# Optimization experiments

Measured on AMD Instinct MI355X. Metric: run time of the kernel, lower is better.

## Reference

```python
import jax, jax.numpy as jnp
import numpy as np

L = 8      # n_layers
D = 512    # msa_dim
P = 128    # pair_dim
H = 8      # n_heads
HD = D // H  # head_dim = 64
B = 2
NS = 4
S = 384


def setup_inputs() -> dict:
    key = jax.random.key(0)
    ks = jax.random.split(key, 24)
    def rn(k, shape, s=0.02):
        return jax.random.normal(k, shape, dtype=jnp.float32) * s
    return {
        "msa_repr": jax.random.normal(ks[0], (B, NS, S, D), dtype=jnp.float32),
        "pair_repr": jax.random.normal(ks[1], (B, S, S, P), dtype=jnp.float32),
        # per-layer IPA params, stacked along layer axis
        "Wq": rn(ks[2], (L, D, D)), "bq": jnp.zeros((L, D), jnp.float32),
        "Wk": rn(ks[3], (L, D, D)), "bk": jnp.zeros((L, D), jnp.float32),
        "Wv": rn(ks[4], (L, D, D)), "bv": jnp.zeros((L, D), jnp.float32),
        "Wpb": rn(ks[5], (L, P, H)), "bpb": jnp.zeros((L, H), jnp.float32),
        "Wo": rn(ks[6], (L, D, D)), "bo": jnp.zeros((L, D), jnp.float32),
        # shared backbone_update MLP (applied after every layer)
        "Wb1": rn(ks[7], (D, D)), "bb1": jnp.zeros((D,), jnp.float32),
        "Wb2": rn(ks[8], (D, 6)), "bb2": jnp.zeros((6,), jnp.float32),
        # confidence head
        "Wc1": rn(ks[9], (D, D // 2)), "bc1": jnp.zeros((D // 2,), jnp.float32),
        "Wc2": rn(ks[10], (D // 2, 1)), "bc2": jnp.zeros((1,), jnp.float32),
    }


def reference(msa_repr, pair_repr, Wq, bq, Wk, bk, Wv, bv, Wpb, bpb, Wo, bo,
              Wb1, bb1, Wb2, bb2, Wc1, bc1, Wc2, bc2):
    Bd, n_seqs, Sd, Dm = msa_repr.shape
    x0 = msa_repr[:, 0]                      # [B,S,D] target sequence repr
    coords0 = jnp.zeros((Bd, Sd, 3), msa_repr.dtype)
    inv_sqrt_hd = jnp.asarray(1.0 / np.sqrt(HD), msa_repr.dtype)

    def layer(carry, p):
        x, coords = carry
        wq, bq_, wk, bk_, wv, bv_, wpb, bpb_, wo, bo_ = p
        q = (x @ wq + bq_).reshape(Bd, Sd, H, HD)
        k = (x @ wk + bk_).reshape(Bd, Sd, H, HD)
        v = (x @ wv + bv_).reshape(Bd, Sd, H, HD)
        scores = jnp.einsum('bihd,bjhd->bhij', q, k) * inv_sqrt_hd
        bias = jnp.einsum('bijp,ph->bhij', pair_repr, wpb) + bpb_[None, :, None, None]
        attn = jax.nn.softmax(scores + bias, axis=-1)   # dropout=0 (eval)
        out = jnp.einsum('bhij,bjhd->bihd', attn, v).reshape(Bd, Sd, Dm)
        x = x + out @ wo + bo_                          # residual
        upd = jax.nn.relu(x @ Wb1 + bb1) @ Wb2 + bb2    # [B,S,6]
        coords = coords + upd[..., :3]                  # translation only
        return (x, coords), None

    (x, coords), _ = jax.lax.scan(layer, (x0, coords0),
                                  (Wq, bq, Wk, bk, Wv, bv, Wpb, bpb, Wo, bo))
    confidence = jax.nn.sigmoid(jax.nn.relu(x @ Wc1 + bc1) @ Wc2 + bc2)[..., 0]
    return coords, confidence
```

## Files before the change

### kernel.cpp

```cpp
#include <hip/hip_runtime.h>
#include <math.h>

#define L 8
#define D 512
#define DD (D*D)
#define P 128
#define H 8
#define HD 64
#define B 2
#define NS 4
#define S 384
#define BS (B*S)
#define XN (BS*D)
#define SS ((size_t)S*S)
#define BHSS ((size_t)B*H*S*S)
#define NSLAB 32

typedef short bf16x8 __attribute__((ext_vector_type(8)));
typedef float f32x4 __attribute__((ext_vector_type(4)));

__device__ __forceinline__ unsigned short f2b(float f) {
    unsigned u = __float_as_uint(f);
    unsigned r = (u + 0x7FFF + ((u >> 16) & 1)) >> 16;
    return (unsigned short)r;
}
__device__ __forceinline__ float b2f(unsigned short u) {
    return __uint_as_float(((unsigned)u) << 16);
}

__global__ __launch_bounds__(256) void k_init(const float* __restrict__ msa,
                                              float* __restrict__ x,
                                              unsigned short* __restrict__ xb,
                                              float* __restrict__ part) {
    int idx = blockIdx.x * 256 + threadIdx.x;
    if (idx < XN) {
        int b = idx / (S * D);
        int rem = idx - b * (S * D);
        float v = msa[(size_t)b * NS * S * D + rem];
        x[idx] = v;
        xb[idx] = f2b(v);
    }
    if (idx < NSLAB * BS * 3) part[idx] = 0.f;
}

__global__ __launch_bounds__(256) void k_prep(const float* __restrict__ Wq,
        const float* __restrict__ Wk, const float* __restrict__ Wv,
        const float* __restrict__ Wo, const float* __restrict__ Wb1,
        const float* __restrict__ Wc1, unsigned short* __restrict__ wt) {
    __shared__ float ts[64][65];
    const int z = blockIdx.z;
    const float* src; int N = 512;
    if (z < 8)       src = Wq + (size_t)z * DD;
    else if (z < 16) src = Wk + (size_t)(z - 8) * DD;
    else if (z < 24) src = Wv + (size_t)(z - 16) * DD;
    else if (z < 32) src = Wo + (size_t)(z - 24) * DD;
    else if (z == 32) src = Wb1;
    else { src = Wc1; N = 256; }
    unsigned short* dst = wt + (size_t)z * DD;

    const int n0 = blockIdx.x * 64, k0 = blockIdx.y * 64;
    if (n0 >= N) return;
    const int t = threadIdx.x;
    #pragma unroll
    for (int m = 0; m < 16; m++) {
        int f = t + m * 256;
        int r = f >> 6, c = f & 63;
        ts[r][c] = src[(size_t)(k0 + r) * N + n0 + c];
    }
    __syncthreads();
    #pragma unroll
    for (int m = 0; m < 4; m++) {
        int o4 = t + m * 256;
        int nr = o4 >> 4, k4 = o4 & 15;
        ushort4 pk;
        pk.x = f2b(ts[k4 * 4 + 0][nr]);
        pk.y = f2b(ts[k4 * 4 + 1][nr]);
        pk.z = f2b(ts[k4 * 4 + 2][nr]);
        pk.w = f2b(ts[k4 * 4 + 3][nr]);
        *(ushort4*)&dst[(size_t)(n0 + nr) * 512 + k0 + k4 * 4] = pk;
    }
}

__global__ __launch_bounds__(256) void k_biasm(const float* __restrict__ pair,
        const float* __restrict__ Wpb, const float* __restrict__ bpb,
        unsigned short* __restrict__ bias) {
    __shared__ unsigned short Ws[64][136];
    __shared__ unsigned short Ps[64][136];
    const int t = threadIdx.x;
    const int lane = t & 63, w = t >> 6;
    const int jt = blockIdx.x, i = blockIdx.y, b = blockIdx.z;

    #pragma unroll
    for (int m = 0; m < 8; m++) {
        int f = (t + m * 256) * 4;
        float4 wv = *(const float4*)&Wpb[f];
        int l = f >> 10, rem = f & 1023;
        int k = rem >> 3, h = rem & 7;
        int lh = (l << 3) | h;
        Ws[lh + 0][k] = f2b(wv.x);
        Ws[lh + 1][k] = f2b(wv.y);
        Ws[lh + 2][k] = f2b(wv.z);
        Ws[lh + 3][k] = f2b(wv.w);
    }
    const float* prow = pair + (((size_t)b * S + i) * S + jt * 64) * P;
    #pragma unroll
    for (int m = 0; m < 8; m++) {
        int f = (t + m * 256) * 4;
        int r = f >> 7, c = f & 127;
        float4 pv = *(const float4*)&prow[f];
        ushort4 u;
        u.x = f2b(pv.x); u.y = f2b(pv.y); u.z = f2b(pv.z); u.w = f2b(pv.w);
        *(ushort4*)&Ps[r][c] = u;
    }
    __syncthreads();

    f32x4 acc[4];
    #pragma unroll
    for (int mi = 0; mi < 4; mi++) { acc[mi][0] = 0.f; acc[mi][1] = 0.f; acc[mi][2] = 0.f; acc[mi][3] = 0.f; }
    #pragma unroll
    for (int ks = 0; ks < 4; ks++) {
        bf16x8 bv = *(const bf16x8*)&Ps[w * 16 + (lane & 15)][ks * 32 + (lane >> 4) * 8];
        #pragma unroll
        for (int mi = 0; mi < 4; mi++) {
            bf16x8 av = *(const bf16x8*)&Ws[mi * 16 + (lane & 15)][ks * 32 + (lane >> 4) * 8];
            acc[mi] = __builtin_amdgcn_mfma_f32_16x16x32_bf16(av, bv, acc[mi], 0, 0, 0);
        }
    }
    const int j = jt * 64 + w * 16 + (lane & 15);
    #pragma unroll
    for (int mi = 0; mi < 4; mi++)
        #pragma unroll
        for (int reg = 0; reg < 4; reg++) {
            int lh = mi * 16 + (lane >> 4) * 4 + reg;
            float v = acc[mi][reg] + bpb[lh];
            size_t plane = ((size_t)(lh >> 3) * B + b) * H + (lh & 7);
            bias[plane * SS + (size_t)i * S + j] = f2b(v);
        }
}

#define GEMM32_CORE(Abase, Wbase)                                              \
    f32x4 acc; acc[0] = 0.f; acc[1] = 0.f; acc[2] = 0.f; acc[3] = 0.f;         \
    {                                                                          \
        const unsigned short* pa = &(Abase)[(size_t)(m0 + sr) * 512 + scc];    \
        const unsigned short* pb = &(Wbase)[(size_t)(n0 + sr) * 512 + scc];    \
        int4 ra = *(const int4*)pa;                                            \
        int4 rb = *(const int4*)pb;                                            \
        *(int4*)&As[0][sr][scc] = ra;                                          \
        *(int4*)&Bs[0][sr][scc] = rb;                                          \
        __syncthreads();                                                       \
        int cur = 0;                                                           \
        for (int kt = 0; kt < 512; kt += 64) {                                 \
            if (kt + 64 < 512) {                                               \
                ra = *(const int4*)(pa + kt + 64);                             \
                rb = *(const int4*)(pb + kt + 64);                             \
            }                                                                  \
            _Pragma("unroll")                                                  \
            for (int kk = 0; kk < 2; kk++) {                                   \
                bf16x8 a = *(const bf16x8*)&As[cur][wr * 16 + (lane & 15)][kk * 32 + (lane >> 4) * 8]; \
                bf16x8 bb = *(const bf16x8*)&Bs[cur][wc * 16 + (lane & 15)][kk * 32 + (lane >> 4) * 8]; \
                acc = __builtin_amdgcn_mfma_f32_16x16x32_bf16(a, bb, acc, 0, 0, 0); \
            }                                                                  \
            if (kt + 64 < 512) {                                               \
                *(int4*)&As[cur ^ 1][sr][scc] = ra;                            \
                *(int4*)&Bs[cur ^ 1][sr][scc] = rb;                            \
            }                                                                  \
            __syncthreads();                                                   \
            cur ^= 1;                                                          \
        }                                                                      \
    }

__global__ __launch_bounds__(256) void k_phaseA(const unsigned short* __restrict__ xb,
        const unsigned short* __restrict__ wt,
        const float* __restrict__ bq, const float* __restrict__ bk, const float* __restrict__ bv,
        unsigned short* __restrict__ qbb, unsigned short* __restrict__ kbb,
        unsigned short* __restrict__ vtb,
        const float* __restrict__ bb1, const float* __restrict__ Wb2g,
        float* __restrict__ part, int l) {
    __shared__ unsigned short As[2][32][72];
    __shared__ unsigned short Bs[2][32][72];
    const int t = threadIdx.x, lane = t & 63;
    const int w = t >> 6, wr = w >> 1, wc = w & 1;
    const int z = blockIdx.z;
    const int m0 = blockIdx.y * 32, n0 = blockIdx.x * 32;
    const int sr = t >> 3, scc = (t & 7) * 8;

    const unsigned short* Wt;
    const float* bias;
    if (z == 0)      { Wt = wt + (size_t)l * DD;        bias = bq + l * D; }
    else if (z == 1) { Wt = wt + (size_t)(8 + l) * DD;  bias = bk + l * D; }
    else if (z == 2) { Wt = wt + (size_t)(16 + l) * DD; bias = bv + l * D; }
    else             { Wt = wt + (size_t)32 * DD;       bias = bb1; }

    GEMM32_CORE(xb, Wt)

    const int col = n0 + wc * 16 + (lane & 15);
    const float bcol = bias[col];
    if (z < 3) {
        unsigned short* out = (z == 0) ? qbb : (z == 1) ? kbb : vtb;
        const int h = col >> 6, d = col & 63;
        #pragma unroll
        for (int reg = 0; reg < 4; reg++) {
            int row = m0 + wr * 16 + (lane >> 4) * 4 + reg;
            int b = row / S, i = row - b * S;
            float v = acc[reg] + bcol;
            if (z < 2) out[(((size_t)b * H + h) * S + i) * HD + d] = f2b(v);
            else       out[(((size_t)b * H + h) * HD + d) * S + i] = f2b(v);
        }
    } else {
        const float w20 = Wb2g[col * 6 + 0];
        const float w21 = Wb2g[col * 6 + 1];
        const float w22 = Wb2g[col * 6 + 2];
        #pragma unroll
        for (int reg = 0; reg < 4; reg++) {
            float v = fmaxf(acc[reg] + bcol, 0.f);
            float p0 = v * w20, p1 = v * w21, p2 = v * w22;
            #pragma unroll
            for (int m = 1; m < 16; m <<= 1) {
                p0 += __shfl_xor(p0, m);
                p1 += __shfl_xor(p1, m);
                p2 += __shfl_xor(p2, m);
            }
            if ((lane & 15) == 0) {
                int row = m0 + wr * 16 + (lane >> 4) * 4 + reg;
                float* pp = &part[((size_t)(blockIdx.x * 2 + wc) * BS + row) * 3];
                pp[0] += p0; pp[1] += p1; pp[2] += p2;
            }
        }
    }
}

__global__ __launch_bounds__(256) void k_wo(const unsigned short* __restrict__ aob,
        const unsigned short* __restrict__ wt, const float* __restrict__ bo,
        float* __restrict__ x, unsigned short* __restrict__ xb, int l) {
    __shared__ unsigned short As[2][32][72];
    __shared__ unsigned short Bs[2][32][72];
    const int t = threadIdx.x, lane = t & 63;
    const int w = t >> 6, wr = w >> 1, wc = w & 1;
    const int m0 = blockIdx.y * 32, n0 = blockIdx.x * 32;
    const int sr = t >> 3, scc = (t & 7) * 8;
    const unsigned short* Wt = wt + (size_t)(24 + l) * DD;

    GEMM32_CORE(aob, Wt)

    const int col = n0 + wc * 16 + (lane & 15);
    const float bcol = bo[l * D + col];
    #pragma unroll
    for (int reg = 0; reg < 4; reg++) {
        int row = m0 + wr * 16 + (lane >> 4) * 4 + reg;
        float v = acc[reg] + bcol + x[(size_t)row * D + col];
        x[(size_t)row * D + col] = v;
        xb[(size_t)row * D + col] = f2b(v);
    }
}

__global__ __launch_bounds__(256) void k_final(const unsigned short* __restrict__ xb,
        const unsigned short* __restrict__ wt,
        const float* __restrict__ bb1, const float* __restrict__ Wb2g, float* __restrict__ part,
        const float* __restrict__ bc1, float* __restrict__ hc) {
    __shared__ unsigned short As[2][32][72];
    __shared__ unsigned short Bs[2][32][72];
    const int t = threadIdx.x, lane = t & 63;
    const int w = t >> 6, wr = w >> 1, wc = w & 1;
    const int z = blockIdx.z;
    if (z == 1 && blockIdx.x >= 8) return;
    const int m0 = blockIdx.y * 32, n0 = blockIdx.x * 32;
    const int sr = t >> 3, scc = (t & 7) * 8;
    const unsigned short* Wt = (z == 0) ? wt + (size_t)32 * DD : wt + (size_t)33 * DD;

    GEMM32_CORE(xb, Wt)

    const int col = n0 + wc * 16 + (lane & 15);
    if (z == 0) {
        const float bcol = bb1[col];
        const float w20 = Wb2g[col * 6 + 0];
        const float w21 = Wb2g[col * 6 + 1];
        const float w22 = Wb2g[col * 6 + 2];
        #pragma unroll
        for (int reg = 0; reg < 4; reg++) {
            float v = fmaxf(acc[reg] + bcol, 0.f);
            float p0 = v * w20, p1 = v * w21, p2 = v * w22;
            #pragma unroll
            for (int m = 1; m < 16; m <<= 1) {
                p0 += __shfl_xor(p0, m);
                p1 += __shfl_xor(p1, m);
                p2 += __shfl_xor(p2, m);
            }
            if ((lane & 15) == 0) {
                int row = m0 + wr * 16 + (lane >> 4) * 4 + reg;
                float* pp = &part[((size_t)(blockIdx.x * 2 + wc) * BS + row) * 3];
                pp[0] += p0; pp[1] += p1; pp[2] += p2;
            }
        }
    } else {
        const float bcol = bc1[col];
        #pragma unroll
        for (int reg = 0; reg < 4; reg++) {
            int row = m0 + wr * 16 + (lane >> 4) * 4 + reg;
            hc[(size_t)row * 256 + col] = fmaxf(acc[reg] + bcol, 0.f);
        }
    }
}

__global__ __launch_bounds__(256) void k_attnm(const unsigned short* __restrict__ qb,
        const unsigned short* __restrict__ kb, const unsigned short* __restrict__ vt,
        const unsigned short* __restrict__ biasL, unsigned short* __restrict__ aob) {
    __shared__ unsigned short qs[16][72];
    __shared__ unsigned short kv[2][64][72];
    __shared__ float scs[16][392];
    __shared__ unsigned short pbs[16][392];
    __shared__ float invs[16];

    const int t = threadIdx.x, lane = t & 63, w = t >> 6;
    const int i0 = blockIdx.x * 16;
    const int h = blockIdx.y, b = blockIdx.z;
    const size_t bh = (size_t)b * H + h;
    const unsigned short* qp = qb + (bh * S + i0) * HD;
    const unsigned short* kp = kb + bh * S * HD;
    const unsigned short* vp = vt + bh * HD * S;
    const unsigned short* bp = biasL + bh * SS + (size_t)i0 * S;

    const int str = t >> 3, stc = (t & 7) * 8;

    if (t < 128) {
        int r = t >> 3, c = (t & 7) * 8;
        *(int4*)&qs[r][c] = *(const int4*)&qp[r * HD + c];
    }
    #pragma unroll
    for (int m = 0; m < 3; m++) {
        int f = t + m * 256;
        int r = f / 48, c = (f % 48) * 8;
        *(int4*)&pbs[r][c] = *(const int4*)&bp[(size_t)r * S + c];
    }
    *(int4*)&kv[0][str][stc]      = *(const int4*)&kp[(size_t)str * HD + stc];
    *(int4*)&kv[0][32 + str][stc] = *(const int4*)&kp[(size_t)(32 + str) * HD + stc];
    __syncthreads();

    bf16x8 qa0 = *(const bf16x8*)&qs[lane & 15][(lane >> 4) * 8];
    bf16x8 qa1 = *(const bf16x8*)&qs[lane & 15][32 + (lane >> 4) * 8];

    int cur = 0;
    for (int jt = 0; jt < 6; jt++) {
        int4 r0, r1;
        if (jt < 5) {
            r0 = *(const int4*)&kp[(size_t)((jt + 1) * 64 + str) * HD + stc];
            r1 = *(const int4*)&kp[(size_t)((jt + 1) * 64 + 32 + str) * HD + stc];
        }
        f32x4 acc; acc[0] = 0.f; acc[1] = 0.f; acc[2] = 0.f; acc[3] = 0.f;
        bf16x8 kb0 = *(const bf16x8*)&kv[cur][w * 16 + (lane & 15)][(lane >> 4) * 8];
        bf16x8 kb1 = *(const bf16x8*)&kv[cur][w * 16 + (lane & 15)][32 + (lane >> 4) * 8];
        acc = __builtin_amdgcn_mfma_f32_16x16x32_bf16(qa0, kb0, acc, 0, 0, 0);
        acc = __builtin_amdgcn_mfma_f32_16x16x32_bf16(qa1, kb1, acc, 0, 0, 0);
        const int col = jt * 64 + w * 16 + (lane & 15);
        #pragma unroll
        for (int reg = 0; reg < 4; reg++) {
            int row = (lane >> 4) * 4 + reg;
            scs[row][col] = acc[reg] * 0.125f + b2f(pbs[row][col]);
        }
        if (jt < 5) {
            *(int4*)&kv[cur ^ 1][str][stc]      = r0;
            *(int4*)&kv[cur ^ 1][32 + str][stc] = r1;
        }
        __syncthreads();
        cur ^= 1;
    }

    int4 v0 = *(const int4*)&vp[(size_t)str * S + stc];
    int4 v1 = *(const int4*)&vp[(size_t)(32 + str) * S + stc];
    const int i = t >> 4, sub = t & 15;
    float mx = -1e30f;
    #pragma unroll
    for (int m = 0; m < 24; m++) mx = fmaxf(mx, scs[i][sub + m * 16]);
    #pragma unroll
    for (int m = 1; m < 16; m <<= 1) mx = fmaxf(mx, __shfl_xor(mx, m));
    float pv_[24];
    float sum = 0.f;
    #pragma unroll
    for (int m = 0; m < 24; m++) {
        float p = __expf(scs[i][sub + m * 16] - mx);
        pv_[m] = p;
        sum += p;
    }
    #pragma unroll
    for (int m = 1; m < 16; m <<= 1) sum += __shfl_xor(sum, m);
    if (sub == 0) invs[i] = 1.f / sum;
    #pragma unroll
    for (int m = 0; m < 24; m++) pbs[i][sub + m * 16] = f2b(pv_[m]);
    *(int4*)&kv[0][str][stc]      = v0;
    *(int4*)&kv[0][32 + str][stc] = v1;
    __syncthreads();

    f32x4 oacc; oacc[0] = 0.f; oacc[1] = 0.f; oacc[2] = 0.f; oacc[3] = 0.f;
    int vc = 0;
    for (int jt = 0; jt < 6; jt++) {
        int4 w0, w1;
        if (jt < 5) {
            w0 = *(const int4*)&vp[(size_t)str * S + (jt + 1) * 64 + stc];
            w1 = *(const int4*)&vp[(size_t)(32 + str) * S + (jt + 1) * 64 + stc];
        }
        #pragma unroll
        for (int kk = 0; kk < 2; kk++) {
            bf16x8 pa = *(const bf16x8*)&pbs[lane & 15][jt * 64 + kk * 32 + (lane >> 4) * 8];
            bf16x8 bb = *(const bf16x8*)&kv[vc][w * 16 + (lane & 15)][kk * 32 + (lane >> 4) * 8];
            oacc = __builtin_amdgcn_mfma_f32_16x16x32_bf16(pa, bb, oacc, 0, 0, 0);
        }
        if (jt < 5) {
            *(int4*)&kv[vc ^ 1][str][stc]      = w0;
            *(int4*)&kv[vc ^ 1][32 + str][stc] = w1;
        }
        __syncthreads();
        vc ^= 1;
    }
    #pragma unroll
    for (int reg = 0; reg < 4; reg++) {
        int row = (lane >> 4) * 4 + reg;
        int d = w * 16 + (lane & 15);
        float v = oacc[reg] * invs[row];
        aob[((size_t)(b * S + i0 + row)) * D + h * HD + d] = f2b(v);
    }
}

__global__ __launch_bounds__(256) void k_conf(const float* __restrict__ hc,
        const float* __restrict__ Wc2, const float* __restrict__ bc2,
        const float* __restrict__ part, const float* __restrict__ bb2,
        float* __restrict__ out) {
    const int wv = threadIdx.x >> 6, lane = threadIdx.x & 63;
    const int row = blockIdx.x * 4 + wv;
    const float* hr = hc + (size_t)row * 256;
    float p = 0.f;
    #pragma unroll
    for (int m = 0; m < 4; m++) p += hr[m * 64 + lane] * Wc2[m * 64 + lane];
    #pragma unroll
    for (int m = 32; m; m >>= 1) p += __shfl_xor(p, m);
    if (lane == 0) out[B * S * 3 + row] = 1.f / (1.f + __expf(-(p + bc2[0])));
    int ci = blockIdx.x * 12 + threadIdx.x;
    if (threadIdx.x < 12) {
        int r = ci / 3, c = ci - r * 3;
        float s = 8.f * bb2[c];
        #pragma unroll
        for (int nb = 0; nb < NSLAB; nb++) s += part[((size_t)nb * BS + r) * 3 + c];
        out[ci] = s;
    }
}

extern "C" void kernel_launch(void* const* d_in, const int* in_sizes, int n_in,
                              void* d_out, int out_size, void* d_ws, size_t ws_size,
                              hipStream_t stream) {
    const float* msa = (const float*)d_in[0];
    const float* pair = (const float*)d_in[1];
    const float* Wq = (const float*)d_in[2];
    const float* bq = (const float*)d_in[3];
    const float* Wk = (const float*)d_in[4];
    const float* bk = (const float*)d_in[5];
    const float* Wv = (const float*)d_in[6];
    const float* bv = (const float*)d_in[7];
    const float* Wpb = (const float*)d_in[8];
    const float* bpb = (const float*)d_in[9];
    const float* Wo = (const float*)d_in[10];
    const float* bo = (const float*)d_in[11];
    const float* Wb1 = (const float*)d_in[12];
    const float* bb1 = (const float*)d_in[13];
    const float* Wb2 = (const float*)d_in[14];
    const float* bb2 = (const float*)d_in[15];
    const float* Wc1 = (const float*)d_in[16];
    const float* bc1 = (const float*)d_in[17];
    const float* Wc2 = (const float*)d_in[18];
    const float* bc2 = (const float*)d_in[19];

    char* base = (char*)d_ws;
    float* x    = (float*)base;            base += (size_t)XN * 4;
    float* hc   = (float*)base;            base += (size_t)BS * 256 * 4;
    float* part = (float*)base;            base += (size_t)NSLAB * BS * 3 * 4;
    unsigned short* xb  = (unsigned short*)base;  base += (size_t)XN * 2;
    unsigned short* aob = (unsigned short*)base;  base += (size_t)XN * 2;
    unsigned short* qbb = (unsigned short*)base;  base += (size_t)XN * 2;
    unsigned short* kbb = (unsigned short*)base;  base += (size_t)XN * 2;
    unsigned short* vtb = (unsigned short*)base;  base += (size_t)XN * 2;
    unsigned short* wt  = (unsigned short*)base;  base += (size_t)34 * DD * 2;
    unsigned short* biasb = (unsigned short*)base;

    k_prep<<<dim3(8, 8, 34), 256, 0, stream>>>(Wq, Wk, Wv, Wo, Wb1, Wc1, wt);
    k_init<<<dim3(1536), 256, 0, stream>>>(msa, x, xb, part);
    k_biasm<<<dim3(6, S, B), 256, 0, stream>>>(pair, Wpb, bpb, biasb);

    for (int l = 0; l < L; ++l) {
        k_phaseA<<<dim3(16, 24, l == 0 ? 3 : 4), 256, 0, stream>>>(xb, wt,
            bq, bk, bv, qbb, kbb, vtb, bb1, Wb2, part, l);
        k_attnm<<<dim3(S / 16, H, B), 256, 0, stream>>>(qbb, kbb, vtb,
            biasb + (size_t)l * BHSS, aob);
        k_wo<<<dim3(16, 24), 256, 0, stream>>>(aob, wt, bo, x, xb, l);
    }

    k_final<<<dim3(16, 24, 2), 256, 0, stream>>>(xb, wt, bb1, Wb2, part, bc1, hc);
    k_conf<<<dim3(BS / 4), 256, 0, stream>>>(hc, Wc2, bc2, part, bb2, (float*)d_out);
}
```

Measured before the change: 252.7 us.

## Use 64x64 tiles in QKV projection GEMM and pre-transpose pair-bias weights

The QKV/backbone projection kernel moves from 32x32 to 64x64 output tiles, with each wave computing a 2x2 grid of MFMA fragments. This raises data reuse per shared-memory load and cuts the block count. Separately, Wpb is converted to a transposed bf16 layout once in the init kernel, so each pair-bias block does a plain vector copy instead of converting and scattering per block. The cost is lower grid parallelism (384 blocks) and more registers per thread.

```diff
diff --git a/kernel.cpp b/kernel.cpp
--- a/kernel.cpp
+++ b/kernel.cpp
@@ -31,7 +31,9 @@
 __global__ __launch_bounds__(256) void k_init(const float* __restrict__ msa,
                                               float* __restrict__ x,
                                               unsigned short* __restrict__ xb,
-                                              float* __restrict__ part) {
+                                              float* __restrict__ part,
+                                              const float* __restrict__ Wpb,
+                                              unsigned short* __restrict__ wpbT) {
     int idx = blockIdx.x * 256 + threadIdx.x;
     if (idx < XN) {
         int b = idx / (S * D);
@@ -41,6 +43,11 @@
         xb[idx] = f2b(v);
     }
     if (idx < NSLAB * BS * 3) part[idx] = 0.f;
+    if (idx < 64 * P) {
+        int l = idx >> 10, rem = idx & 1023;
+        int p = rem >> 3, h = rem & 7;
+        wpbT[(size_t)((l << 3) | h) * P + p] = f2b(Wpb[idx]);
+    }
 }
 
 __global__ __launch_bounds__(256) void k_prep(const float* __restrict__ Wq,
@@ -82,7 +89,7 @@
 }
 
 __global__ __launch_bounds__(256) void k_biasm(const float* __restrict__ pair,
-        const float* __restrict__ Wpb, const float* __restrict__ bpb,
+        const unsigned short* __restrict__ wpbT, const float* __restrict__ bpb,
         unsigned short* __restrict__ bias) {
     __shared__ unsigned short Ws[64][136];
     __shared__ unsigned short Ps[64][136];
@@ -91,16 +98,10 @@
     const int jt = blockIdx.x, i = blockIdx.y, b = blockIdx.z;
 
     #pragma unroll
-    for (int m = 0; m < 8; m++) {
-        int f = (t + m * 256) * 4;
-        float4 wv = *(const float4*)&Wpb[f];
-        int l = f >> 10, rem = f & 1023;
-        int k = rem >> 3, h = rem & 7;
-        int lh = (l << 3) | h;
-        Ws[lh + 0][k] = f2b(wv.x);
-        Ws[lh + 1][k] = f2b(wv.y);
-        Ws[lh + 2][k] = f2b(wv.z);
-        Ws[lh + 3][k] = f2b(wv.w);
+    for (int m = 0; m < 4; m++) {
+        int f = t + m * 256;
+        int r = f >> 4, c8 = f & 15;
+        *(int4*)&Ws[r][c8 * 8] = *(const int4*)&wpbT[(size_t)r * P + c8 * 8];
     }
     const float* prow = pair + (((size_t)b * S + i) * S + jt * 64) * P;
     #pragma unroll
@@ -137,6 +138,55 @@
             bias[plane * SS + (size_t)i * S + j] = f2b(v);
         }
 }
+
+#define GEMM64_CORE(Abase, Wbase)                                              \
+    f32x4 acc[2][2];                                                           \
+    _Pragma("unroll")                                                          \
+    for (int qz = 0; qz < 2; qz++)                                             \
+        _Pragma("unroll")                                                      \
+        for (int rz = 0; rz < 2; rz++) {                                       \
+            acc[qz][rz][0] = 0.f; acc[qz][rz][1] = 0.f;                        \
+            acc[qz][rz][2] = 0.f; acc[qz][rz][3] = 0.f;                        \
+        }                                                                      \
+    {                                                                          \
+        const unsigned short* pa0 = &(Abase)[(size_t)(m0 + srow) * 512 + sc0]; \
+        const unsigned short* pa1 = pa0 + 32 * 512;                            \
+        const unsigned short* pb0 = &(Wbase)[(size_t)(n0 + srow) * 512 + sc0]; \
+        const unsigned short* pb1 = pb0 + 32 * 512;                            \
+        int4 ra0 = *(const int4*)pa0, ra1 = *(const int4*)pa1;                 \
+        int4 rb0 = *(const int4*)pb0, rb1 = *(const int4*)pb1;                 \
+        *(int4*)&As[0][srow][sc0] = ra0;  *(int4*)&As[0][srow + 32][sc0] = ra1;\
+        *(int4*)&Bs[0][srow][sc0] = rb0;  *(int4*)&Bs[0][srow + 32][sc0] = rb1;\
+        __syncthreads();                                                       \
+        int cur = 0;                                                           \
+        for (int kt = 0; kt < 512; kt += 64) {                                 \
+            if (kt + 64 < 512) {                                               \
+                ra0 = *(const int4*)(pa0 + kt + 64);                           \
+                ra1 = *(const int4*)(pa1 + kt + 64);                           \
+                rb0 = *(const int4*)(pb0 + kt + 64);                           \
+                rb1 = *(const int4*)(pb1 + kt + 64);                           \
+            }                                                                  \
+            _Pragma("unroll")                                                  \
+            for (int kk = 0; kk < 2; kk++) {                                   \
+                bf16x8 a0 = *(const bf16x8*)&As[cur][wr * 32 + (lane & 15)][kk * 32 + (lane >> 4) * 8];      \
+                bf16x8 a1 = *(const bf16x8*)&As[cur][wr * 32 + 16 + (lane & 15)][kk * 32 + (lane >> 4) * 8]; \
+                bf16x8 b0 = *(const bf16x8*)&Bs[cur][wc * 32 + (lane & 15)][kk * 32 + (lane >> 4) * 8];      \
+                bf16x8 b1 = *(const bf16x8*)&Bs[cur][wc * 32 + 16 + (lane & 15)][kk * 32 + (lane >> 4) * 8]; \
+                acc[0][0] = __builtin_amdgcn_mfma_f32_16x16x32_bf16(a0, b0, acc[0][0], 0, 0, 0); \
+                acc[0][1] = __builtin_amdgcn_mfma_f32_16x16x32_bf16(a0, b1, acc[0][1], 0, 0, 0); \
+                acc[1][0] = __builtin_amdgcn_mfma_f32_16x16x32_bf16(a1, b0, acc[1][0], 0, 0, 0); \
+                acc[1][1] = __builtin_amdgcn_mfma_f32_16x16x32_bf16(a1, b1, acc[1][1], 0, 0, 0); \
+            }                                                                  \
+            if (kt + 64 < 512) {                                               \
+                *(int4*)&As[cur ^ 1][srow][sc0] = ra0;                         \
+                *(int4*)&As[cur ^ 1][srow + 32][sc0] = ra1;                    \
+                *(int4*)&Bs[cur ^ 1][srow][sc0] = rb0;                         \
+                *(int4*)&Bs[cur ^ 1][srow + 32][sc0] = rb1;                    \
+            }                                                                  \
+            __syncthreads();                                                   \
+            cur ^= 1;                                                          \
+        }                                                                      \
+    }
 
 #define GEMM32_CORE(Abase, Wbase)                                              \
     f32x4 acc; acc[0] = 0.f; acc[1] = 0.f; acc[2] = 0.f; acc[3] = 0.f;         \
@@ -176,13 +226,13 @@
         unsigned short* __restrict__ vtb,
         const float* __restrict__ bb1, const float* __restrict__ Wb2g,
         float* __restrict__ part, int l) {
-    __shared__ unsigned short As[2][32][72];
-    __shared__ unsigned short Bs[2][32][72];
+    __shared__ unsigned short As[2][64][72];
+    __shared__ unsigned short Bs[2][64][72];
     const int t = threadIdx.x, lane = t & 63;
     const int w = t >> 6, wr = w >> 1, wc = w & 1;
     const int z = blockIdx.z;
-    const int m0 = blockIdx.y * 32, n0 = blockIdx.x * 32;
-    const int sr = t >> 3, scc = (t & 7) * 8;
+    const int m0 = blockIdx.y * 64, n0 = blockIdx.x * 64;
+    const int srow = t >> 3, sc0 = (t & 7) * 8;
 
     const unsigned short* Wt;
     const float* bias;
@@ -191,41 +241,58 @@
     else if (z == 2) { Wt = wt + (size_t)(16 + l) * DD; bias = bv + l * D; }
     else             { Wt = wt + (size_t)32 * DD;       bias = bb1; }
 
-    GEMM32_CORE(xb, Wt)
-
-    const int col = n0 + wc * 16 + (lane & 15);
-    const float bcol = bias[col];
+    GEMM64_CORE(xb, Wt)
+
     if (z < 3) {
         unsigned short* out = (z == 0) ? qbb : (z == 1) ? kbb : vtb;
-        const int h = col >> 6, d = col & 63;
-        #pragma unroll
-        for (int reg = 0; reg < 4; reg++) {
-            int row = m0 + wr * 16 + (lane >> 4) * 4 + reg;
-            int b = row / S, i = row - b * S;
-            float v = acc[reg] + bcol;
-            if (z < 2) out[(((size_t)b * H + h) * S + i) * HD + d] = f2b(v);
-            else       out[(((size_t)b * H + h) * HD + d) * S + i] = f2b(v);
+        #pragma unroll
+        for (int ac = 0; ac < 2; ac++) {
+            int col = n0 + wc * 32 + ac * 16 + (lane & 15);
+            float bcol = bias[col];
+            int h = col >> 6, d = col & 63;
+            #pragma unroll
+            for (int ar = 0; ar < 2; ar++)
+                #pragma unroll
+                for (int reg = 0; reg < 4; reg++) {
+                    int row = m0 + wr * 32 + ar * 16 + (lane >> 4) * 4 + reg;
+                    int b = row / S, i = row - b * S;
+                    float v = acc[ar][ac][reg] + bcol;
+                    if (z < 2) out[(((size_t)b * H + h) * S + i) * HD + d] = f2b(v);
+                    else       out[(((size_t)b * H + h) * HD + d) * S + i] = f2b(v);
+                }
         }
     } else {
-        const float w20 = Wb2g[col * 6 + 0];
-        const float w21 = Wb2g[col * 6 + 1];
-        const float w22 = Wb2g[col * 6 + 2];
-        #pragma unroll
-        for (int reg = 0; reg < 4; reg++) {
-            float v = fmaxf(acc[reg] + bcol, 0.f);
-            float p0 = v * w20, p1 = v * w21, p2 = v * w22;
+        float bc[2], w20[2], w21[2], w22[2];
+        #pragma unroll
+        for (int ac = 0; ac < 2; ac++) {
+            int col = n0 + wc * 32 + ac * 16 + (lane & 15);
+            bc[ac] = bias[col];
+            w20[ac] = Wb2g[col * 6 + 0];
+            w21[ac] = Wb2g[col * 6 + 1];
+            w22[ac] = Wb2g[col * 6 + 2];
+        }
+        #pragma unroll
+        for (int ar = 0; ar < 2; ar++)
             #pragma unroll
-            for (int m = 1; m < 16; m <<= 1) {
-                p0 += __shfl_xor(p0, m);
-                p1 += __shfl_xor(p1, m);
-                p2 += __shfl_xor(p2, m);
+            for (int reg = 0; reg < 4; reg++) {
+                float p0 = 0.f, p1 = 0.f, p2 = 0.f;
+                #pragma unroll
+                for (int ac = 0; ac < 2; ac++) {
+                    float v = fmaxf(acc[ar][ac][reg] + bc[ac], 0.f);
+                    p0 += v * w20[ac]; p1 += v * w21[ac]; p2 += v * w22[ac];
+                }
+                #pragma unroll
+                for (int m = 1; m < 16; m <<= 1) {
+                    p0 += __shfl_xor(p0, m);
+                    p1 += __shfl_xor(p1, m);
+                    p2 += __shfl_xor(p2, m);
+                }
+                if ((lane & 15) == 0) {
+                    int row = m0 + wr * 32 + ar * 16 + (lane >> 4) * 4 + reg;
+                    float* pp = &part[((size_t)(blockIdx.x * 2 + wc) * BS + row) * 3];
+                    pp[0] += p0; pp[1] += p1; pp[2] += p2;
+                }
             }
-            if ((lane & 15) == 0) {
-                int row = m0 + wr * 16 + (lane >> 4) * 4 + reg;
-                float* pp = &part[((size_t)(blockIdx.x * 2 + wc) * BS + row) * 3];
-                pp[0] += p0; pp[1] += p1; pp[2] += p2;
-            }
-        }
     }
 }
 
@@ -476,14 +543,15 @@
     unsigned short* kbb = (unsigned short*)base;  base += (size_t)XN * 2;
     unsigned short* vtb = (unsigned short*)base;  base += (size_t)XN * 2;
     unsigned short* wt  = (unsigned short*)base;  base += (size_t)34 * DD * 2;
+    unsigned short* wpbT = (unsigned short*)base; base += (size_t)64 * P * 2;
     unsigned short* biasb = (unsigned short*)base;
 
     k_prep<<<dim3(8, 8, 34), 256, 0, stream>>>(Wq, Wk, Wv, Wo, Wb1, Wc1, wt);
-    k_init<<<dim3(1536), 256, 0, stream>>>(msa, x, xb, part);
-    k_biasm<<<dim3(6, S, B), 256, 0, stream>>>(pair, Wpb, bpb, biasb);
+    k_init<<<dim3(1536), 256, 0, stream>>>(msa, x, xb, part, Wpb, wpbT);
+    k_biasm<<<dim3(6, S, B), 256, 0, stream>>>(pair, wpbT, bpb, biasb);
 
     for (int l = 0; l < L; ++l) {
-        k_phaseA<<<dim3(16, 24, l == 0 ? 3 : 4), 256, 0, stream>>>(xb, wt,
+        k_phaseA<<<dim3(8, 12, l == 0 ? 3 : 4), 256, 0, stream>>>(xb, wt,
             bq, bk, bv, qbb, kbb, vtb, bb1, Wb2, part, l);
         k_attnm<<<dim3(S / 16, H, B), 256, 0, stream>>>(qbb, kbb, vtb,
             biasb + (size_t)l * BHSS, aob);
```

After: 255.6 us. No clear change (+1.2%).
